# Kernel tuning notes

Hardware: AMD Instinct MI355X
Metric: run time of the kernel (lower is better)

Reference implementation:

```python
import jax, jax.numpy as jnp
import numpy as np

B, C, H, W = 4, 64, 64, 64
CI = C // 2  # inter_channels


def setup_inputs() -> dict:
    key = jax.random.key(0)
    k1, k2, k3, k4, k5 = jax.random.split(key, 5)
    x = jax.random.normal(k1, (B, C, H, W), dtype=jnp.float32)
    # 1x1 conv g: in C -> CI (weight [CI, C], bias [CI])
    Wg = jax.random.normal(k2, (CI, C), dtype=jnp.float32) * (1.0 / np.sqrt(C))
    bg = jax.random.normal(k3, (CI,), dtype=jnp.float32) * 0.01
    # 1x1 conv W_z: CI -> C
    Wz = jax.random.normal(k4, (C, CI), dtype=jnp.float32) * (1.0 / np.sqrt(CI))
    bz = jax.random.normal(k5, (C,), dtype=jnp.float32) * 0.01
    return {"x": x, "Wg": Wg, "bg": bg, "Wz": Wz, "bz": bz}


def reference(x, Wg, bg, Wz, bz):
    b, c, h, w = x.shape
    n = h * w
    xf = x.reshape(b, c, n)                       # [B,C,N]
    # g projection (1x1 conv) then flatten: [B,N,CI]
    g_x = jnp.einsum('bcn,oc->bno', xf, Wg) + bg  # [B,N,CI]
    # theta = phi = raw x flattened
    theta = xf.transpose(0, 2, 1)                 # [B,N,C]
    f = jnp.einsum('bnc,bcm->bnm', theta, xf)     # [B,N,N]
    f_div_C = jax.nn.softmax(f, axis=-1)
    y = jnp.einsum('bnm,bmo->bno', f_div_C, g_x)  # [B,N,CI]
    y = y.transpose(0, 2, 1).reshape(b, CI, h, w)  # [B,CI,H,W]
    # W_z projection (1x1 conv) + residual
    W_y = jnp.einsum('oi,bihw->bohw', Wz, y) + bz[None, :, None, None]
    return W_y + x
```

## Files before the change

### kernel.cpp

```cpp
#include <hip/hip_runtime.h>
#include <hip/hip_bf16.h>
#include <math.h>

#define B_  4
#define C_  64
#define N_  4096
#define CI_ 32

typedef __attribute__((ext_vector_type(8))) unsigned short u16x8;
typedef __attribute__((ext_vector_type(8))) __bf16        bf16x8;
typedef __attribute__((ext_vector_type(4))) float         f32x4;

__device__ __forceinline__ unsigned short f2bf(float f) {
    union { float f; unsigned int i; } v; v.f = f;
    unsigned int r = v.i + 0x7FFFu + ((v.i >> 16) & 1u);
    return (unsigned short)(r >> 16);
}

__global__ __launch_bounds__(256) void k_prep(
    const float* __restrict__ x, const float* __restrict__ Wg,
    const float* __restrict__ bg, unsigned short* __restrict__ xT,
    unsigned short* __restrict__ gx, float* __restrict__ diag)
{
    __shared__ __align__(16) float tile[64][68];
    __shared__ float part[4][64][33];
    const int t  = threadIdx.x;
    const int b  = blockIdx.x >> 6;
    const int n0 = (blockIdx.x & 63) * 64;

    #pragma unroll
    for (int pass = 0; pass < 4; ++pass) {
        int c   = (t >> 4) + pass * 16;
        int nl4 = (t & 15) * 4;
        float4 v = *(const float4*)(x + (size_t)(b * C_ + c) * N_ + n0 + nl4);
        *(float4*)&tile[c][nl4] = v;
    }
    __syncthreads();

    {
        const int n  = t >> 2;
        const int cc = (t & 3) * 16;
        u16x8 a, b2;
        #pragma unroll
        for (int j = 0; j < 8; ++j) a[j]  = f2bf(tile[cc + j][n]);
        #pragma unroll
        for (int j = 0; j < 8; ++j) b2[j] = f2bf(tile[cc + 8 + j][n]);
        unsigned short* dst = xT + (size_t)(b * N_ + n0 + n) * C_ + cc;
        *(u16x8*)dst       = a;
        *(u16x8*)(dst + 8) = b2;
    }
    {
        const int nl = t & 63, cq = t >> 6;
        float acc[CI_];
        #pragma unroll
        for (int o = 0; o < CI_; ++o) acc[o] = 0.f;
        float dd = 0.f;
        #pragma unroll 4
        for (int cl = 0; cl < 16; ++cl) {
            int c = cq * 16 + cl;
            float xv = tile[c][nl];
            dd += xv * xv;
            #pragma unroll
            for (int o = 0; o < CI_; ++o) acc[o] += Wg[o * C_ + c] * xv;
        }
        #pragma unroll
        for (int o = 0; o < CI_; ++o) part[cq][nl][o] = acc[o];
        part[cq][nl][32] = dd;
    }
    __syncthreads();
    {
        const int o = t >> 3, nr = (t & 7) * 8;
        u16x8 w;
        #pragma unroll
        for (int j = 0; j < 8; ++j) {
            int n = nr + j;
            float s = part[0][n][o] + part[1][n][o] + part[2][n][o] + part[3][n][o]
                    + bg[o];
            w[j] = f2bf(s);
        }
        *(u16x8*)(gx + (size_t)(b * CI_ + o) * N_ + n0 + nr) = w;
    }
    if (t < 64)
        diag[(size_t)b * N_ + n0 + t] =
            part[0][t][32] + part[1][t][32] + part[2][t][32] + part[3][t][32];
}

__device__ __forceinline__ f32x4 mfma16(bf16x8 a, bf16x8 b, f32x4 c) {
    return __builtin_amdgcn_mfma_f32_16x16x32_bf16(a, b, c, 0, 0, 0);
}

__global__ __launch_bounds__(256, 4) void k_flash(
    const unsigned short* __restrict__ xT, const unsigned short* __restrict__ gx,
    const float* __restrict__ diag,
    float* __restrict__ ypart, float* __restrict__ lpart)
{
    __shared__ __align__(16) char smem[24576];
    unsigned short* xk = (unsigned short*)smem;
    unsigned short* vt = (unsigned short*)(smem + 9216);
    unsigned short* Pl = (unsigned short*)(smem + 14336);

    const int tid  = threadIdx.x;
    const int wave = tid >> 6, lane = tid & 63;
    const int quad = lane >> 4, li = lane & 15;
    const int g = wave >> 1, qh = wave & 1;
    const int bi  = blockIdx.x;
    const int kq  = bi & 3;
    const int qtb = (bi >> 2) & 63;
    const int b   = bi >> 8;
    const int qw  = qtb * 64 + qh * 32;
    const int u   = tid & 127;

    float Kq[2];
    #pragma unroll
    for (int qt = 0; qt < 2; ++qt)
        Kq[qt] = diag[(size_t)b * N_ + qw + qt * 16 + li];

    bf16x8 Qf[2][2];
    #pragma unroll
    for (int qt = 0; qt < 2; ++qt)
        #pragma unroll
        for (int kc = 0; kc < 2; ++kc)
            Qf[qt][kc] = *(const bf16x8*)(xT + (size_t)(b * N_ + qw + qt * 16 + li) * C_
                                          + kc * 32 + quad * 8);

    f32x4 Yf[2][2];
    #pragma unroll
    for (int qt = 0; qt < 2; ++qt)
        #pragma unroll
        for (int ot = 0; ot < 2; ++ot)
            Yf[qt][ot] = (f32x4){0.f, 0.f, 0.f, 0.f};
    float lacc[2] = {0.f, 0.f};

    const int keybase = kq * 1024 + g * 512;

    for (int tl = 0; tl < 16; ++tl) {
        const int k0 = keybase + tl * 32;
        __syncthreads();
        #pragma unroll
        for (int j = 0; j < 2; ++j) {
            int cc2 = u * 2 + j;
            int key = cc2 >> 3, coff = (cc2 & 7) * 8;
            *(u16x8*)(xk + (g * 32 + key) * 72 + coff) =
                *(const u16x8*)(xT + (size_t)(b * N_ + k0 + key) * C_ + coff);
        }
        {
            int o = u >> 2, koff = (u & 3) * 8;
            *(u16x8*)(vt + (g * 32 + o) * 40 + koff) =
                *(const u16x8*)(gx + (size_t)(b * CI_ + o) * N_ + k0 + koff);
        }
        __syncthreads();

        bf16x8 A[2][2];
        #pragma unroll
        for (int kt = 0; kt < 2; ++kt)
            #pragma unroll
            for (int kc = 0; kc < 2; ++kc)
                A[kt][kc] = *(const bf16x8*)(xk + (g * 32 + kt * 16 + li) * 72
                                             + kc * 32 + quad * 8);
        f32x4 S[2][2];
        #pragma unroll
        for (int kt = 0; kt < 2; ++kt)
            #pragma unroll
            for (int qt = 0; qt < 2; ++qt) {
                f32x4 z = (f32x4){0.f, 0.f, 0.f, 0.f};
                z = mfma16(A[kt][0], Qf[qt][0], z);
                S[kt][qt] = mfma16(A[kt][1], Qf[qt][1], z);
            }

        #pragma unroll
        for (int qt = 0; qt < 2; ++qt) {
            float p[2][4];
            #pragma unroll
            for (int kt = 0; kt < 2; ++kt)
                #pragma unroll
                for (int r = 0; r < 4; ++r) {
                    p[kt][r] = __expf(S[kt][qt][r] - Kq[qt]);
                    lacc[qt] += p[kt][r];
                }
            #pragma unroll
            for (int kt = 0; kt < 2; ++kt) {
                uint2 wv;
                wv.x = (unsigned)f2bf(p[kt][0]) | ((unsigned)f2bf(p[kt][1]) << 16);
                wv.y = (unsigned)f2bf(p[kt][2]) | ((unsigned)f2bf(p[kt][3]) << 16);
                *(uint2*)(Pl + (wave * 32 + qt * 16 + li) * 40 + kt * 16 + quad * 4) = wv;
            }
        }

        bf16x8 Ap[2], Bv[2];
        #pragma unroll
        for (int qt = 0; qt < 2; ++qt)
            Ap[qt] = *(const bf16x8*)(Pl + (wave * 32 + qt * 16 + li) * 40 + quad * 8);
        #pragma unroll
        for (int ot = 0; ot < 2; ++ot)
            Bv[ot] = *(const bf16x8*)(vt + (g * 32 + ot * 16 + li) * 40 + quad * 8);
        #pragma unroll
        for (int qt = 0; qt < 2; ++qt)
            #pragma unroll
            for (int ot = 0; ot < 2; ++ot)
                Yf[qt][ot] = mfma16(Ap[qt], Bv[ot], Yf[qt][ot]);
    }

    #pragma unroll
    for (int qt = 0; qt < 2; ++qt) {
        lacc[qt] += __shfl_xor(lacc[qt], 16, 64);
        lacc[qt] += __shfl_xor(lacc[qt], 32, 64);
    }

    __syncthreads();
    float* ym = (float*)smem;

    #pragma unroll
    for (int qt = 0; qt < 2; ++qt) {
        #pragma unroll
        for (int ot = 0; ot < 2; ++ot)
            #pragma unroll
            for (int r = 0; r < 4; ++r)
                ym[(wave * 32 + qt * 16 + quad * 4 + r) * 34 + ot * 16 + li] = Yf[qt][ot][r];
        if (quad == 0)
            ym[(wave * 32 + qt * 16 + li) * 34 + 32] = lacc[qt];
    }
    __syncthreads();
    {
        const int q = tid >> 2, og = tid & 3;
        const int qh2 = q >> 5, ql = q & 31;
        const int w0 = qh2, w1 = 2 + qh2;
        const size_t pbase = (size_t)(b * 64 + qtb) * 4 + kq;
        float* yp = ypart + pbase * 2048 + q * 32;
        #pragma unroll
        for (int j = 0; j < 8; ++j) {
            int o = og * 8 + j;
            yp[o] = ym[(w0 * 32 + ql) * 34 + o] + ym[(w1 * 32 + ql) * 34 + o];
        }
        if (og == 0)
            lpart[pbase * 64 + q] = ym[(w0 * 32 + ql) * 34 + 32]
                                  + ym[(w1 * 32 + ql) * 34 + 32];
    }
}

__global__ __launch_bounds__(256) void k_merge(
    const float* __restrict__ ypart, const float* __restrict__ lpart,
    const float* __restrict__ x, const float* __restrict__ Wz,
    const float* __restrict__ bz, float* __restrict__ out)
{
    __shared__ float yfin[64][33];
    const int t   = threadIdx.x;
    const int b   = blockIdx.x >> 6;
    const int qtb = blockIdx.x & 63;
    const int q0  = qtb * 64;

    {
        const int q = t >> 2, og = t & 3;
        const size_t pb = (size_t)(b * 64 + qtb) * 4;
        float l = lpart[(pb + 0) * 64 + q] + lpart[(pb + 1) * 64 + q]
                + lpart[(pb + 2) * 64 + q] + lpart[(pb + 3) * 64 + q];
        float inv = 1.f / l;
        #pragma unroll
        for (int j = 0; j < 8; ++j) {
            int o = og * 8 + j;
            float acc = 0.f;
            #pragma unroll
            for (int kq = 0; kq < 4; ++kq)
                acc += ypart[(pb + kq) * 2048 + q * 32 + o];
            yfin[q][o] = acc * inv;
        }
    }
    __syncthreads();
    {
        const int q = t & 63, c0 = t >> 6;
        #pragma unroll
        for (int i = 0; i < 16; ++i) {
            int cout = c0 + i * 4;
            float acc = bz[cout];
            #pragma unroll
            for (int o = 0; o < CI_; ++o)
                acc += Wz[cout * CI_ + o] * yfin[q][o];
            size_t oidx = (size_t)(b * C_ + cout) * N_ + q0 + q;
            out[oidx] = acc + x[oidx];
        }
    }
}

extern "C" void kernel_launch(void* const* d_in, const int* in_sizes, int n_in,
                              void* d_out, int out_size, void* d_ws, size_t ws_size,
                              hipStream_t stream) {
    (void)in_sizes; (void)n_in; (void)out_size; (void)ws_size;
    const float* x  = (const float*)d_in[0];
    const float* Wg = (const float*)d_in[1];
    const float* bg = (const float*)d_in[2];
    const float* Wz = (const float*)d_in[3];
    const float* bz = (const float*)d_in[4];
    float* out = (float*)d_out;

    unsigned short* xT = (unsigned short*)d_ws;
    unsigned short* gx = (unsigned short*)((char*)d_ws + 2097152);
    float* diag  = (float*)((char*)d_ws + 3145728);
    float* ypart = (float*)((char*)d_ws + 3211264);
    float* lpart = (float*)((char*)d_ws + 11599872);

    hipLaunchKernelGGL(k_prep,  dim3(B_ * (N_ / 64)),    dim3(256), 0, stream, x, Wg, bg, xT, gx, diag);
    hipLaunchKernelGGL(k_flash, dim3(B_ * 64 * 4),       dim3(256), 0, stream, xT, gx, diag, ypart, lpart);
    hipLaunchKernelGGL(k_merge, dim3(B_ * 64),           dim3(256), 0, stream, ypart, lpart, x, Wz, bz, out);
}
```

Measured before the change: 117.9 us.

## Load K/V fragments directly from global and widen each wave to 64 queries

The flash kernel no longer stages key and value tiles through shared memory with two block barriers per iteration. Each wave now reads its MFMA operand fragments straight from global memory (L2/L1) and owns a private 256-key range. Each wave now covers all 64 queries of the block instead of 32, and the four per-wave partials are reduced in shared memory at the end. This removes the barrier and LDS-copy overhead, at the cost of more registers (launch bounds lowered to 3 blocks), a larger LDS footprint, and more global load traffic with less reuse.

New measurement: 122.1 us. +3.6%, slower.

```diff
diff --git a/kernel.cpp b/kernel.cpp
--- a/kernel.cpp
+++ b/kernel.cpp
@@ -89,86 +89,78 @@
     return __builtin_amdgcn_mfma_f32_16x16x32_bf16(a, b, c, 0, 0, 0);
 }
 
-__global__ __launch_bounds__(256, 4) void k_flash(
+__global__ __launch_bounds__(256, 3) void k_flash(
     const unsigned short* __restrict__ xT, const unsigned short* __restrict__ gx,
     const float* __restrict__ diag,
     float* __restrict__ ypart, float* __restrict__ lpart)
 {
-    __shared__ __align__(16) char smem[24576];
-    unsigned short* xk = (unsigned short*)smem;
-    unsigned short* vt = (unsigned short*)(smem + 9216);
-    unsigned short* Pl = (unsigned short*)(smem + 14336);
+    __shared__ __align__(16) char smem[34816];
+    unsigned short* Pl = (unsigned short*)smem;
+    float*          ym = (float*)smem;
 
     const int tid  = threadIdx.x;
     const int wave = tid >> 6, lane = tid & 63;
     const int quad = lane >> 4, li = lane & 15;
-    const int g = wave >> 1, qh = wave & 1;
     const int bi  = blockIdx.x;
     const int kq  = bi & 3;
     const int qtb = (bi >> 2) & 63;
     const int b   = bi >> 8;
-    const int qw  = qtb * 64 + qh * 32;
-    const int u   = tid & 127;
-
-    float Kq[2];
-    #pragma unroll
-    for (int qt = 0; qt < 2; ++qt)
-        Kq[qt] = diag[(size_t)b * N_ + qw + qt * 16 + li];
-
-    bf16x8 Qf[2][2];
-    #pragma unroll
-    for (int qt = 0; qt < 2; ++qt)
+    const int q0  = qtb * 64;
+
+    const unsigned short* xTb = xT + (size_t)b * N_ * C_;
+    const unsigned short* gxb = gx + (size_t)(b * CI_) * N_;
+
+    float Kq[4];
+    #pragma unroll
+    for (int qt = 0; qt < 4; ++qt)
+        Kq[qt] = diag[(size_t)b * N_ + q0 + qt * 16 + li];
+
+    bf16x8 Qf[4][2];
+    #pragma unroll
+    for (int qt = 0; qt < 4; ++qt)
         #pragma unroll
         for (int kc = 0; kc < 2; ++kc)
-            Qf[qt][kc] = *(const bf16x8*)(xT + (size_t)(b * N_ + qw + qt * 16 + li) * C_
+            Qf[qt][kc] = *(const bf16x8*)(xTb + (size_t)(q0 + qt * 16 + li) * C_
                                           + kc * 32 + quad * 8);
 
-    f32x4 Yf[2][2];
-    #pragma unroll
-    for (int qt = 0; qt < 2; ++qt)
+    f32x4 Yf[4][2];
+    #pragma unroll
+    for (int qt = 0; qt < 4; ++qt)
         #pragma unroll
         for (int ot = 0; ot < 2; ++ot)
             Yf[qt][ot] = (f32x4){0.f, 0.f, 0.f, 0.f};
-    float lacc[2] = {0.f, 0.f};
-
-    const int keybase = kq * 1024 + g * 512;
-
-    for (int tl = 0; tl < 16; ++tl) {
+    float lacc[4] = {0.f, 0.f, 0.f, 0.f};
+
+    const int keybase = kq * 1024 + wave * 256;
+
+    for (int tl = 0; tl < 8; ++tl) {
         const int k0 = keybase + tl * 32;
-        __syncthreads();
-        #pragma unroll
-        for (int j = 0; j < 2; ++j) {
-            int cc2 = u * 2 + j;
-            int key = cc2 >> 3, coff = (cc2 & 7) * 8;
-            *(u16x8*)(xk + (g * 32 + key) * 72 + coff) =
-                *(const u16x8*)(xT + (size_t)(b * N_ + k0 + key) * C_ + coff);
-        }
-        {
-            int o = u >> 2, koff = (u & 3) * 8;
-            *(u16x8*)(vt + (g * 32 + o) * 40 + koff) =
-                *(const u16x8*)(gx + (size_t)(b * CI_ + o) * N_ + k0 + koff);
-        }
-        __syncthreads();
 
         bf16x8 A[2][2];
         #pragma unroll
         for (int kt = 0; kt < 2; ++kt)
             #pragma unroll
             for (int kc = 0; kc < 2; ++kc)
-                A[kt][kc] = *(const bf16x8*)(xk + (g * 32 + kt * 16 + li) * 72
+                A[kt][kc] = *(const bf16x8*)(xTb + (size_t)(k0 + kt * 16 + li) * C_
                                              + kc * 32 + quad * 8);
-        f32x4 S[2][2];
+        bf16x8 Bv[2];
+        #pragma unroll
+        for (int ot = 0; ot < 2; ++ot)
+            Bv[ot] = *(const bf16x8*)(gxb + (size_t)(ot * 16 + li) * N_
+                                      + k0 + quad * 8);
+
+        f32x4 S[2][4];
         #pragma unroll
         for (int kt = 0; kt < 2; ++kt)
             #pragma unroll
-            for (int qt = 0; qt < 2; ++qt) {
+            for (int qt = 0; qt < 4; ++qt) {
                 f32x4 z = (f32x4){0.f, 0.f, 0.f, 0.f};
                 z = mfma16(A[kt][0], Qf[qt][0], z);
                 S[kt][qt] = mfma16(A[kt][1], Qf[qt][1], z);
             }
 
         #pragma unroll
-        for (int qt = 0; qt < 2; ++qt) {
+        for (int qt = 0; qt < 4; ++qt) {
             float p[2][4];
             #pragma unroll
             for (int kt = 0; kt < 2; ++kt)
@@ -182,58 +174,50 @@
                 uint2 wv;
                 wv.x = (unsigned)f2bf(p[kt][0]) | ((unsigned)f2bf(p[kt][1]) << 16);
                 wv.y = (unsigned)f2bf(p[kt][2]) | ((unsigned)f2bf(p[kt][3]) << 16);
-                *(uint2*)(Pl + (wave * 32 + qt * 16 + li) * 40 + kt * 16 + quad * 4) = wv;
+                *(uint2*)(Pl + (wave * 64 + qt * 16 + li) * 40 + kt * 16 + quad * 4) = wv;
             }
         }
 
-        bf16x8 Ap[2], Bv[2];
-        #pragma unroll
-        for (int qt = 0; qt < 2; ++qt)
-            Ap[qt] = *(const bf16x8*)(Pl + (wave * 32 + qt * 16 + li) * 40 + quad * 8);
-        #pragma unroll
-        for (int ot = 0; ot < 2; ++ot)
-            Bv[ot] = *(const bf16x8*)(vt + (g * 32 + ot * 16 + li) * 40 + quad * 8);
-        #pragma unroll
-        for (int qt = 0; qt < 2; ++qt)
+        #pragma unroll
+        for (int qt = 0; qt < 4; ++qt) {
+            bf16x8 Ap = *(const bf16x8*)(Pl + (wave * 64 + qt * 16 + li) * 40 + quad * 8);
             #pragma unroll
             for (int ot = 0; ot < 2; ++ot)
-                Yf[qt][ot] = mfma16(Ap[qt], Bv[ot], Yf[qt][ot]);
-    }
-
-    #pragma unroll
-    for (int qt = 0; qt < 2; ++qt) {
+                Yf[qt][ot] = mfma16(Ap, Bv[ot], Yf[qt][ot]);
+        }
+    }
+
+    #pragma unroll
+    for (int qt = 0; qt < 4; ++qt) {
         lacc[qt] += __shfl_xor(lacc[qt], 16, 64);
         lacc[qt] += __shfl_xor(lacc[qt], 32, 64);
     }
 
     __syncthreads();
-    float* ym = (float*)smem;
-
-    #pragma unroll
-    for (int qt = 0; qt < 2; ++qt) {
+    #pragma unroll
+    for (int qt = 0; qt < 4; ++qt) {
         #pragma unroll
         for (int ot = 0; ot < 2; ++ot)
             #pragma unroll
             for (int r = 0; r < 4; ++r)
-                ym[(wave * 32 + qt * 16 + quad * 4 + r) * 34 + ot * 16 + li] = Yf[qt][ot][r];
+                ym[(wave * 64 + qt * 16 + quad * 4 + r) * 34 + ot * 16 + li] = Yf[qt][ot][r];
         if (quad == 0)
-            ym[(wave * 32 + qt * 16 + li) * 34 + 32] = lacc[qt];
+            ym[(wave * 64 + qt * 16 + li) * 34 + 32] = lacc[qt];
     }
     __syncthreads();
     {
         const int q = tid >> 2, og = tid & 3;
-        const int qh2 = q >> 5, ql = q & 31;
-        const int w0 = qh2, w1 = 2 + qh2;
         const size_t pbase = (size_t)(b * 64 + qtb) * 4 + kq;
         float* yp = ypart + pbase * 2048 + q * 32;
         #pragma unroll
         for (int j = 0; j < 8; ++j) {
             int o = og * 8 + j;
-            yp[o] = ym[(w0 * 32 + ql) * 34 + o] + ym[(w1 * 32 + ql) * 34 + o];
+            yp[o] = ym[(0 * 64 + q) * 34 + o] + ym[(1 * 64 + q) * 34 + o]
+                  + ym[(2 * 64 + q) * 34 + o] + ym[(3 * 64 + q) * 34 + o];
         }
         if (og == 0)
-            lpart[pbase * 64 + q] = ym[(w0 * 32 + ql) * 34 + 32]
-                                  + ym[(w1 * 32 + ql) * 34 + 32];
+            lpart[pbase * 64 + q] = ym[(0 * 64 + q) * 34 + 32] + ym[(1 * 64 + q) * 34 + 32]
+                                  + ym[(2 * 64 + q) * 34 + 32] + ym[(3 * 64 + q) * 34 + 32];
     }
 }
 
@@ -297,7 +281,7 @@
     float* ypart = (float*)((char*)d_ws + 3211264);
     float* lpart = (float*)((char*)d_ws + 11599872);
 
-    hipLaunchKernelGGL(k_prep,  dim3(B_ * (N_ / 64)),    dim3(256), 0, stream, x, Wg, bg, xT, gx, diag);
-    hipLaunchKernelGGL(k_flash, dim3(B_ * 64 * 4),       dim3(256), 0, stream, xT, gx, diag, ypart, lpart);
-    hipLaunchKernelGGL(k_merge, dim3(B_ * 64),           dim3(256), 0, stream, ypart, lpart, x, Wz, bz, out);
-}
+    hipLaunchKernelGGL(k_prep,  dim3(B_ * (N_ / 64)), dim3(256), 0, stream, x, Wg, bg, xT, gx, diag);
+    hipLaunchKernelGGL(k_flash, dim3(B_ * 64 * 4),    dim3(256), 0, stream, xT, gx, diag, ypart, lpart);
+    hipLaunchKernelGGL(k_merge, dim3(B_ * 64),        dim3(256), 0, stream, ypart, lpart, x, Wz, bz, out);
+}
```
